# Performance work log

Measured on AMD Instinct MI355X. Metric: run time of the kernel, lower is better.

## Reference

```python
import jax, jax.numpy as jnp
import numpy as np

K3 = 27            # kernel_size**3
PAIRS_PER_K = 131072  # pairs per kernel offset (equal-size segments)
N_VOX = 262144     # active voxels (stride-1, same grid: N_in == N_out)
C_IN = 32
C_OUT = 32


def setup_inputs() -> dict:
    key = jax.random.key(0)
    k1, k2, k3, k4 = jax.random.split(key, 4)
    M = K3 * PAIRS_PER_K
    in_feature = jax.random.normal(k1, (N_VOX, C_IN), dtype=jnp.float32)
    kernel = jax.random.normal(k2, (K3, C_IN, C_OUT), dtype=jnp.float32) * (1.0 / np.sqrt(C_IN * K3))
    bias = jax.random.normal(k3, (C_OUT,), dtype=jnp.float32) * 0.01
    # nbmap[:, 0] = input voxel index, nbmap[:, 1] = output voxel index,
    # sorted by kernel offset (offset k owns rows [k*P, (k+1)*P)).
    nbmap = jax.random.randint(k4, (M, 2), 0, N_VOX, dtype=jnp.int32)
    nbsizes = jnp.full((K3,), PAIRS_PER_K, dtype=jnp.int32)
    return {"in_feature": in_feature, "kernel": kernel, "bias": bias,
            "nbmap": nbmap, "nbsizes": nbsizes}


def reference(in_feature, kernel, bias, nbmap, nbsizes):
    """Gather -> per-offset GEMM -> scatter-add, matching
    ext.conv.sparse_convolution for a stride-1 non-transposed conv where
    nbmap rows are grouped by kernel offset with equal segment sizes."""
    k3, c_in, c_out = kernel.shape
    m = nbmap.shape[0]
    p = m // k3  # pairs per offset (static)
    n_out = in_feature.shape[0]  # same grid, stride 1
    # gather input features for every (input, output) pair  [M, C_in]
    gathered = in_feature[nbmap[:, 0]]
    # batched GEMM: one [P, C_in] x [C_in, C_out] per kernel offset
    contrib = jnp.einsum('kpi,kio->kpo', gathered.reshape(k3, p, c_in), kernel)
    contrib = contrib.reshape(m, c_out)
    # scatter-add contributions into output voxels
    out = jax.ops.segment_sum(contrib, nbmap[:, 1], num_segments=n_out)
    return out + bias
```

## Files before the change

kernel.cpp:

```cpp
#include <hip/hip_runtime.h>
#include <hip/hip_bf16.h>


#define N_VOX    262144
#define LOG2_NV  18
#define C_CH     32
#define K3       27
#define LOG2_PPK 17
#define BLOCK    256
#define FLAG_FIN 0x40000000
#define ECAP     4096
#define PLPAD    36
#define FRAGN    (K3 * 2 * 64)

typedef __attribute__((ext_vector_type(8))) short bf16x8;
typedef __attribute__((ext_vector_type(4))) float f32x4;

__device__ __forceinline__ unsigned short f2bf(float f) {
  union { __hip_bfloat16 h; unsigned short u; } cv;
  cv.h = __float2bfloat16(f);
  return cv.u;
}

__global__ __launch_bounds__(BLOCK) void passA_kernel(
    const int4* __restrict__ nbmap2, int* __restrict__ T, int Mh) {
  int q = blockIdx.x * BLOCK + threadIdx.x;
  if (q >= Mh) return;
  int4 nb = nbmap2[q];
  int p0 = q << 1, p1 = (q << 1) | 1;
  T[((p0 >> LOG2_PPK) << LOG2_NV) + nb.y] = p0;
  T[((p1 >> LOG2_PPK) << LOG2_NV) + nb.w] = p1;
}

__device__ __forceinline__ void loser_path(
    int vox, int k, int in, int* __restrict__ T2, int idx, int use2,
    int* __restrict__ ovf_cnt, int* __restrict__ ovf, int S2,
    int* __restrict__ ecnt, int2* __restrict__ elist) {
  int val = in;
  if (use2) {
    val = atomicExch(&T2[idx], val);
    if (val < 0) return;
  }
  int pos = atomicAdd(&ovf_cnt[vox], 1);
  if (pos < S2) {
    ovf[(pos << LOG2_NV) + vox] = (k << LOG2_NV) | val;
  } else {
    int ep = atomicAdd(ecnt, 1);
    if (ep < ECAP) elist[ep] = make_int2(vox, (k << LOG2_NV) | val);
  }
}

__global__ __launch_bounds__(BLOCK) void passB_kernel(
    const int4* __restrict__ nbmap2, int* __restrict__ T, int* __restrict__ T2,
    int use2, int* __restrict__ ovf_cnt, int* __restrict__ ovf, int S2,
    int* __restrict__ ecnt, int2* __restrict__ elist, int Mh) {
  int q = blockIdx.x * BLOCK + threadIdx.x;
  if (q >= Mh) return;
  int4 nb = nbmap2[q];
  int p0 = q << 1, p1 = (q << 1) | 1;
  int k0 = p0 >> LOG2_PPK, k1 = p1 >> LOG2_PPK;
  int idx0 = (k0 << LOG2_NV) + nb.y;
  int idx1 = (k1 << LOG2_NV) + nb.w;
  int t0 = T[idx0];
  int t1 = T[idx1];
  if (t0 == p0) {
    T[idx0] = FLAG_FIN | nb.x;
  } else {
    loser_path(nb.y, k0, nb.x, T2, idx0, use2, ovf_cnt, ovf, S2, ecnt, elist);
  }
  if (t1 == p1) {
    T[idx1] = FLAG_FIN | nb.z;
  } else {
    loser_path(nb.w, k1, nb.z, T2, idx1, use2, ovf_cnt, ovf, S2, ecnt, elist);
  }
}

__global__ __launch_bounds__(BLOCK) void bf_prep_kernel(
    const float* __restrict__ kernel_w, unsigned short* __restrict__ Bf) {
  int tid = blockIdx.x * BLOCK + threadIdx.x;
  if (tid >= FRAGN) return;
  int lane = tid & 63;
  int kc = tid >> 6;
  int k = kc >> 1, t = kc & 1;
  int i0 = (lane >> 4) * 8;
  int c = t * 16 + (lane & 15);
  union { unsigned short u[8]; uint4 v; } pk;
#pragma unroll
  for (int j = 0; j < 8; ++j)
    pk.u[j] = f2bf(kernel_w[(k << 10) + (i0 + j) * C_CH + c]);
  ((uint4*)Bf)[tid] = pk.v;
}

__global__ __launch_bounds__(BLOCK) void feat16_prep_kernel(
    const float* __restrict__ in_feature, unsigned short* __restrict__ feat16) {
  int idx = blockIdx.x * BLOCK + threadIdx.x;
  const float4* src = (const float4*)in_feature + (idx << 1);
  float4 f0 = src[0], f1 = src[1];
  union { unsigned short u[8]; uint4 v; } pk;
  pk.u[0] = f2bf(f0.x); pk.u[1] = f2bf(f0.y);
  pk.u[2] = f2bf(f0.z); pk.u[3] = f2bf(f0.w);
  pk.u[4] = f2bf(f1.x); pk.u[5] = f2bf(f1.y);
  pk.u[6] = f2bf(f1.z); pk.u[7] = f2bf(f1.w);
  ((uint4*)feat16)[idx] = pk.v;
}

template <int F16>
__global__ __launch_bounds__(BLOCK, 4) void gather_splitk_kernel(
    const float* __restrict__ in_feature,
    const unsigned short* __restrict__ feat16,
    const float* __restrict__ kernel_w,
    const float* __restrict__ bias,
    const int* __restrict__ T,
    const int* __restrict__ T2, int use2,
    const int* __restrict__ ovf_cnt,
    const int* __restrict__ ovf,
    const unsigned short* __restrict__ Bf,
    float* __restrict__ out, int S2) {
  __shared__ float plane[4][16][PLPAD];
  __shared__ int flatE[256];
  __shared__ int scnt[16];

  const int tid = threadIdx.x;
  const int w = tid >> 6;
  const int lane = tid & 63;
  const int r16 = lane & 15;
  const int quad = lane >> 4;
  const int vb = blockIdx.x << 4;

  if (tid < 16) {
    int c = ovf_cnt[vb + tid];
    scnt[tid] = c < S2 ? c : S2;
  }
  __syncthreads();
  const int er = tid & 15;
  const int ej = tid >> 4;
  int myb = 0, tot = 0;
#pragma unroll
  for (int q = 0; q < 16; ++q) {
    int cq = scnt[q];
    if (q < er) myb += cq;
    tot += cq;
  }
  if (ej < scnt[er])
    flatE[myb + ej] = (er << 24) | ovf[(ej << LOG2_NV) + vb + er];
  __syncthreads();

  const int kb = w * 7;
  const int kn = (w == 3) ? 6 : 7;
  const int v = vb + r16;
  int tv[7], tv2[7];
#pragma unroll
  for (int d = 0; d < 7; ++d)
    tv[d] = (d < kn) ? T[((kb + d) << LOG2_NV) + v] : -1;
#pragma unroll
  for (int d = 0; d < 7; ++d)
    tv2[d] = (use2 && d < kn) ? T2[((kb + d) << LOG2_NV) + v] : -1;

  bf16x8 R0[7], R1[7];
#pragma unroll
  for (int d = 0; d < 7; ++d) {
    int t = tv[d];
    int in = (t >= 0) ? (t & 0x3FFFF) : 0;
    bf16x8 a;
    if (F16) {
      a = *reinterpret_cast<const bf16x8*>(feat16 + (in << 5) + (quad << 3));
    } else {
      const float4* ap = (const float4*)(in_feature + (in << 5) + (quad << 3));
      float4 f0 = ap[0], f1 = ap[1];
      a[0] = (short)f2bf(f0.x); a[1] = (short)f2bf(f0.y);
      a[2] = (short)f2bf(f0.z); a[3] = (short)f2bf(f0.w);
      a[4] = (short)f2bf(f1.x); a[5] = (short)f2bf(f1.y);
      a[6] = (short)f2bf(f1.z); a[7] = (short)f2bf(f1.w);
    }
    if (t < 0) a = (bf16x8)0;
    R0[d] = a;
  }
#pragma unroll
  for (int d = 0; d < 7; ++d) {
    int t = tv2[d];
    int in = (t >= 0) ? (t & 0x3FFFF) : 0;
    bf16x8 a;
    if (F16) {
      a = *reinterpret_cast<const bf16x8*>(feat16 + (in << 5) + (quad << 3));
    } else {
      const float4* ap = (const float4*)(in_feature + (in << 5) + (quad << 3));
      float4 f0 = ap[0], f1 = ap[1];
      a[0] = (short)f2bf(f0.x); a[1] = (short)f2bf(f0.y);
      a[2] = (short)f2bf(f0.z); a[3] = (short)f2bf(f0.w);
      a[4] = (short)f2bf(f1.x); a[5] = (short)f2bf(f1.y);
      a[6] = (short)f2bf(f1.z); a[7] = (short)f2bf(f1.w);
    }
    if (t < 0) a = (bf16x8)0;
    R1[d] = a;
  }

  f32x4 acc0 = {0.f, 0.f, 0.f, 0.f};
  f32x4 acc1 = {0.f, 0.f, 0.f, 0.f};
  const uint4* bfp = (const uint4*)Bf;
#pragma unroll
  for (int d = 0; d < 7; ++d) {
    if (d < kn) {
      int k = kb + d;
      uint4 h0 = bfp[(k * 2 + 0) * 64 + lane];
      uint4 h1 = bfp[(k * 2 + 1) * 64 + lane];
      acc0 = __builtin_amdgcn_mfma_f32_16x16x32_bf16(
          R0[d], *reinterpret_cast<const bf16x8*>(&h0), acc0, 0, 0, 0);
      acc1 = __builtin_amdgcn_mfma_f32_16x16x32_bf16(
          R0[d], *reinterpret_cast<const bf16x8*>(&h1), acc1, 0, 0, 0);
    }
  }
  if (use2) {
#pragma unroll
    for (int d = 0; d < 7; ++d) {
      if (d < kn) {
        int k = kb + d;
        uint4 h0 = bfp[(k * 2 + 0) * 64 + lane];
        uint4 h1 = bfp[(k * 2 + 1) * 64 + lane];
        acc0 = __builtin_amdgcn_mfma_f32_16x16x32_bf16(
            R1[d], *reinterpret_cast<const bf16x8*>(&h0), acc0, 0, 0, 0);
        acc1 = __builtin_amdgcn_mfma_f32_16x16x32_bf16(
            R1[d], *reinterpret_cast<const bf16x8*>(&h1), acc1, 0, 0, 0);
      }
    }
  }

#pragma unroll
  for (int reg = 0; reg < 4; ++reg) {
    int row = quad * 4 + reg;
    plane[w][row][r16] = acc0[reg];
    plane[w][row][16 + r16] = acc1[reg];
  }

  const int c32 = lane & 31, h = lane >> 5;
  int i = w;
  int e_cur = 0;
  float4 p0, p1, p2, p3;
  if (i < tot) {
    e_cur = flatE[i];
    const float4* ar =
        (const float4*)(in_feature + ((e_cur & 0x3FFFF) << 5) + (h << 4));
    p0 = ar[0]; p1 = ar[1]; p2 = ar[2]; p3 = ar[3];
  }
  while (i < tot) {
    const int e = e_cur;
    float4 q0 = p0, q1 = p1, q2 = p2, q3 = p3;
    const int inext = i + 4;
    if (inext < tot) {
      e_cur = flatE[inext];
      const float4* ar =
          (const float4*)(in_feature + ((e_cur & 0x3FFFF) << 5) + (h << 4));
      p0 = ar[0]; p1 = ar[1]; p2 = ar[2]; p3 = ar[3];
    }
    const int k2 = (e >> LOG2_NV) & 31;
    const int rr = (e >> 24) & 15;
    const float* wcol = kernel_w + (k2 << 10) + (h << 4) * C_CH + c32;
    float psum = 0.f;
    psum = fmaf(q0.x, wcol[0 * C_CH], psum);
    psum = fmaf(q0.y, wcol[1 * C_CH], psum);
    psum = fmaf(q0.z, wcol[2 * C_CH], psum);
    psum = fmaf(q0.w, wcol[3 * C_CH], psum);
    psum = fmaf(q1.x, wcol[4 * C_CH], psum);
    psum = fmaf(q1.y, wcol[5 * C_CH], psum);
    psum = fmaf(q1.z, wcol[6 * C_CH], psum);
    psum = fmaf(q1.w, wcol[7 * C_CH], psum);
    psum = fmaf(q2.x, wcol[8 * C_CH], psum);
    psum = fmaf(q2.y, wcol[9 * C_CH], psum);
    psum = fmaf(q2.z, wcol[10 * C_CH], psum);
    psum = fmaf(q2.w, wcol[11 * C_CH], psum);
    psum = fmaf(q3.x, wcol[12 * C_CH], psum);
    psum = fmaf(q3.y, wcol[13 * C_CH], psum);
    psum = fmaf(q3.z, wcol[14 * C_CH], psum);
    psum = fmaf(q3.w, wcol[15 * C_CH], psum);
    psum += __shfl_xor(psum, 32);
    if (h == 0) plane[w][rr][c32] += psum;
    i = inext;
  }

  __syncthreads();
  const int mr = tid >> 4;
  const int mc = (tid & 15) << 1;
  float s0 = plane[0][mr][mc] + plane[1][mr][mc] + plane[2][mr][mc] +
             plane[3][mr][mc] + bias[mc];
  float s1 = plane[0][mr][mc + 1] + plane[1][mr][mc + 1] +
             plane[2][mr][mc + 1] + plane[3][mr][mc + 1] + bias[mc + 1];
  float2 o; o.x = s0; o.y = s1;
  *(float2*)(out + ((vb + mr) << 5) + mc) = o;
}

__global__ __launch_bounds__(BLOCK) void emergency_kernel(
    const float* __restrict__ in_feature, const float* __restrict__ kernel_w,
    const int* __restrict__ ecnt, const int2* __restrict__ elist,
    float* __restrict__ out) {
  int e = blockIdx.x * BLOCK + threadIdx.x;
  int n = *ecnt;
  if (n > ECAP) n = ECAP;
  if (e >= n) return;
  int2 ent = elist[e];
  int v = ent.x, k = ent.y >> LOG2_NV, in = ent.y & 0x3FFFF;
  float a[C_CH];
  const float4* ar = (const float4*)(in_feature + (in << 5));
#pragma unroll
  for (int q = 0; q < 8; ++q) ((float4*)a)[q] = ar[q];
  for (int c = 0; c < C_CH; ++c) {
    float s = 0.f;
#pragma unroll
    for (int i = 0; i < C_CH; ++i)
      s = fmaf(a[i], kernel_w[(k << 10) + i * C_CH + c], s);
    atomicAdd(&out[v * C_CH + c], s);
  }
}

__global__ __launch_bounds__(BLOCK) void init_bias_kernel(
    float* __restrict__ out, const float* __restrict__ bias, int n4) {
  int idx = blockIdx.x * blockDim.x + threadIdx.x;
  if (idx >= n4) return;
  ((float4*)out)[idx] = ((const float4*)bias)[idx & 7];
}

__global__ __launch_bounds__(BLOCK) void scatter_conv_kernel(
    const float* __restrict__ in_feature, const float* __restrict__ kernel_w,
    const int* __restrict__ nbmap, float* __restrict__ out) {
  const int k = blockIdx.x >> 9;
  const int pair = blockIdx.x * BLOCK + threadIdx.x;
  const float* __restrict__ Wk = kernel_w + k * (C_CH * C_CH);
  const int2 nb = ((const int2*)nbmap)[pair];
  const float4* __restrict__ inrow =
      (const float4*)(in_feature + (long)nb.x * C_CH);
  float a[C_CH];
#pragma unroll
  for (int j = 0; j < 8; ++j) ((float4*)a)[j] = inrow[j];
  float acc[C_CH];
#pragma unroll
  for (int c = 0; c < C_CH; ++c) acc[c] = 0.0f;
#pragma unroll
  for (int i = 0; i < C_CH; ++i) {
    const float av = a[i];
#pragma unroll
    for (int c = 0; c < C_CH; ++c)
      acc[c] = fmaf(av, Wk[i * C_CH + c], acc[c]);
  }
  float* __restrict__ orow = out + (long)nb.y * C_CH;
#pragma unroll
  for (int c = 0; c < C_CH; ++c) atomicAdd(orow + c, acc[c]);
}

extern "C" void kernel_launch(void* const* d_in, const int* in_sizes, int n_in,
                              void* d_out, int out_size, void* d_ws,
                              size_t ws_size, hipStream_t stream) {
  const float* in_feature = (const float*)d_in[0];
  const float* kernel_w   = (const float*)d_in[1];
  const float* bias       = (const float*)d_in[2];
  const int*   nbmap      = (const int*)d_in[3];
  float* out = (float*)d_out;
  const int M = in_sizes[3] / 2;
  const int Mh = M / 2;

  const long FIXED = 64 + 2 * ECAP + 13824;
  long ws_ints = (long)(ws_size / 4);
  long planes = (ws_ints - FIXED) / N_VOX;
  int use2 = 0, use16 = 0;
  long s2c;
  if (planes >= 75) {
    use2 = 1; use16 = 1;
    s2c = planes - 71;
    if (s2c > 7) s2c = 7;
  } else if (planes >= 59) {
    use2 = 1;
    s2c = planes - 55;
    if (s2c > 7) s2c = 7;
  } else {
    s2c = planes - 28;
    if (s2c > 15) s2c = 15;
  }
  int S2 = (int)s2c;

  if (!use2 && S2 < 4) {
    const int n4 = out_size / 4;
    init_bias_kernel<<<(n4 + BLOCK - 1) / BLOCK, BLOCK, 0, stream>>>(out, bias,
                                                                     n4);
    scatter_conv_kernel<<<M / BLOCK, BLOCK, 0, stream>>>(in_feature, kernel_w,
                                                         nbmap, out);
    return;
  }

  const long TPLANES = (long)K3 * N_VOX;
  int* T        = (int*)d_ws;
  int* T2       = use2 ? (T + TPLANES) : T;
  int* ovf_cnt  = T + TPLANES * (1 + use2);
  int* ecnt     = ovf_cnt + N_VOX;
  int2* elist   = (int2*)(ecnt + 64);
  unsigned short* Bf = (unsigned short*)(ecnt + 64 + 2 * ECAP);
  int* ovf      = ((int*)Bf) + 13824;
  unsigned short* feat16 = (unsigned short*)(ovf + (long)S2 * N_VOX);

  hipMemsetAsync(T, 0xFF, (size_t)TPLANES * 4 * (1 + use2), stream);
  hipMemsetAsync(ovf_cnt, 0, (size_t)(N_VOX + 64) * 4, stream);

  bf_prep_kernel<<<(FRAGN + BLOCK - 1) / BLOCK, BLOCK, 0, stream>>>(kernel_w,
                                                                    Bf);
  if (use16)
    feat16_prep_kernel<<<(N_VOX * 4) / BLOCK, BLOCK, 0, stream>>>(in_feature,
                                                                  feat16);
  passA_kernel<<<(Mh + BLOCK - 1) / BLOCK, BLOCK, 0, stream>>>(
      (const int4*)nbmap, T, Mh);
  passB_kernel<<<(Mh + BLOCK - 1) / BLOCK, BLOCK, 0, stream>>>(
      (const int4*)nbmap, T, T2, use2, ovf_cnt, ovf, S2, ecnt, elist, Mh);
  if (use16)
    gather_splitk_kernel<1><<<N_VOX / 16, BLOCK, 0, stream>>>(
        in_feature, feat16, kernel_w, bias, T, T2, use2, ovf_cnt, ovf, Bf,
        out, S2);
  else
    gather_splitk_kernel<0><<<N_VOX / 16, BLOCK, 0, stream>>>(
        in_feature, feat16, kernel_w, bias, T, T2, use2, ovf_cnt, ovf, Bf,
        out, S2);
  emergency_kernel<<<ECAP / BLOCK, BLOCK, 0, stream>>>(in_feature, kernel_w,
                                                       ecnt, elist, out);
}
```

Before: 389.1 us.

## Fuse setup memsets and prep kernels, widen pass work, hoist gather loads

Two memsets and the bf16 weight and feature prep kernels become one setup kernel that clears the T planes and counters and converts features and weights, removing several launches. passA and passB now handle four pairs per thread instead of two, which gives more memory-level parallelism per thread and halves the thread count. In the gather kernel, the overflow-list load and the T-plane loads are issued before the first barrier so their latency overlaps the count reduction. Risks are a larger, divergent setup grid and more register pressure in the pass kernels.

```diff
diff --git a/kernel.cpp b/kernel.cpp
--- a/kernel.cpp
+++ b/kernel.cpp
@@ -12,6 +12,7 @@
 #define ECAP     4096
 #define PLPAD    36
 #define FRAGN    (K3 * 2 * 64)
+#define NF16     (N_VOX * 4)
 
 typedef __attribute__((ext_vector_type(8))) short bf16x8;
 typedef __attribute__((ext_vector_type(4))) float f32x4;
@@ -22,14 +23,62 @@
   return cv.u;
 }
 
+__global__ __launch_bounds__(BLOCK) void setup_kernel(
+    int4* __restrict__ clrT, long nt4, int4* __restrict__ clrC, long nc4,
+    const float* __restrict__ in_feature, unsigned short* __restrict__ feat16,
+    int use16, const float* __restrict__ kernel_w,
+    unsigned short* __restrict__ Bf) {
+  long idx = (long)blockIdx.x * BLOCK + threadIdx.x;
+  if (idx < nt4) {
+    clrT[idx] = make_int4(-1, -1, -1, -1);
+    return;
+  }
+  idx -= nt4;
+  if (idx < nc4) {
+    clrC[idx] = make_int4(0, 0, 0, 0);
+    return;
+  }
+  idx -= nc4;
+  if (use16) {
+    if (idx < NF16) {
+      const float4* src = (const float4*)in_feature + (idx << 1);
+      float4 f0 = src[0], f1 = src[1];
+      union { unsigned short u[8]; uint4 v; } pk;
+      pk.u[0] = f2bf(f0.x); pk.u[1] = f2bf(f0.y);
+      pk.u[2] = f2bf(f0.z); pk.u[3] = f2bf(f0.w);
+      pk.u[4] = f2bf(f1.x); pk.u[5] = f2bf(f1.y);
+      pk.u[6] = f2bf(f1.z); pk.u[7] = f2bf(f1.w);
+      ((uint4*)feat16)[idx] = pk.v;
+      return;
+    }
+    idx -= NF16;
+  }
+  if (idx < FRAGN) {
+    int wid = (int)idx;
+    int lane = wid & 63;
+    int kc = wid >> 6;
+    int k = kc >> 1, t = kc & 1;
+    int i0 = (lane >> 4) * 8;
+    int c = t * 16 + (lane & 15);
+    union { unsigned short u[8]; uint4 v; } pk;
+#pragma unroll
+    for (int j = 0; j < 8; ++j)
+      pk.u[j] = f2bf(kernel_w[(k << 10) + (i0 + j) * C_CH + c]);
+    ((uint4*)Bf)[wid] = pk.v;
+  }
+}
+
 __global__ __launch_bounds__(BLOCK) void passA_kernel(
-    const int4* __restrict__ nbmap2, int* __restrict__ T, int Mh) {
+    const int4* __restrict__ nbmap2, int* __restrict__ T, int Mq) {
   int q = blockIdx.x * BLOCK + threadIdx.x;
-  if (q >= Mh) return;
-  int4 nb = nbmap2[q];
-  int p0 = q << 1, p1 = (q << 1) | 1;
-  T[((p0 >> LOG2_PPK) << LOG2_NV) + nb.y] = p0;
-  T[((p1 >> LOG2_PPK) << LOG2_NV) + nb.w] = p1;
+  if (q >= Mq) return;
+  int4 na = nbmap2[q * 2];
+  int4 nb = nbmap2[q * 2 + 1];
+  int p0 = q << 2, p1 = p0 | 1, p2 = p0 | 2, p3 = p0 | 3;
+  T[((p0 >> LOG2_PPK) << LOG2_NV) + na.y] = p0;
+  T[((p1 >> LOG2_PPK) << LOG2_NV) + na.w] = p1;
+  T[((p2 >> LOG2_PPK) << LOG2_NV) + nb.y] = p2;
+  T[((p3 >> LOG2_PPK) << LOG2_NV) + nb.w] = p3;
 }
 
 __device__ __forceinline__ void loser_path(
@@ -53,55 +102,32 @@
 __global__ __launch_bounds__(BLOCK) void passB_kernel(
     const int4* __restrict__ nbmap2, int* __restrict__ T, int* __restrict__ T2,
     int use2, int* __restrict__ ovf_cnt, int* __restrict__ ovf, int S2,
-    int* __restrict__ ecnt, int2* __restrict__ elist, int Mh) {
+    int* __restrict__ ecnt, int2* __restrict__ elist, int Mq) {
   int q = blockIdx.x * BLOCK + threadIdx.x;
-  if (q >= Mh) return;
-  int4 nb = nbmap2[q];
-  int p0 = q << 1, p1 = (q << 1) | 1;
-  int k0 = p0 >> LOG2_PPK, k1 = p1 >> LOG2_PPK;
-  int idx0 = (k0 << LOG2_NV) + nb.y;
-  int idx1 = (k1 << LOG2_NV) + nb.w;
+  if (q >= Mq) return;
+  int4 na = nbmap2[q * 2];
+  int4 nb = nbmap2[q * 2 + 1];
+  int p0 = q << 2, p1 = p0 | 1, p2 = p0 | 2, p3 = p0 | 3;
+  int idx0 = ((p0 >> LOG2_PPK) << LOG2_NV) + na.y;
+  int idx1 = ((p1 >> LOG2_PPK) << LOG2_NV) + na.w;
+  int idx2 = ((p2 >> LOG2_PPK) << LOG2_NV) + nb.y;
+  int idx3 = ((p3 >> LOG2_PPK) << LOG2_NV) + nb.w;
   int t0 = T[idx0];
   int t1 = T[idx1];
-  if (t0 == p0) {
-    T[idx0] = FLAG_FIN | nb.x;
-  } else {
-    loser_path(nb.y, k0, nb.x, T2, idx0, use2, ovf_cnt, ovf, S2, ecnt, elist);
-  }
-  if (t1 == p1) {
-    T[idx1] = FLAG_FIN | nb.z;
-  } else {
-    loser_path(nb.w, k1, nb.z, T2, idx1, use2, ovf_cnt, ovf, S2, ecnt, elist);
-  }
-}
-
-__global__ __launch_bounds__(BLOCK) void bf_prep_kernel(
-    const float* __restrict__ kernel_w, unsigned short* __restrict__ Bf) {
-  int tid = blockIdx.x * BLOCK + threadIdx.x;
-  if (tid >= FRAGN) return;
-  int lane = tid & 63;
-  int kc = tid >> 6;
-  int k = kc >> 1, t = kc & 1;
-  int i0 = (lane >> 4) * 8;
-  int c = t * 16 + (lane & 15);
-  union { unsigned short u[8]; uint4 v; } pk;
-#pragma unroll
-  for (int j = 0; j < 8; ++j)
-    pk.u[j] = f2bf(kernel_w[(k << 10) + (i0 + j) * C_CH + c]);
-  ((uint4*)Bf)[tid] = pk.v;
-}
-
-__global__ __launch_bounds__(BLOCK) void feat16_prep_kernel(
-    const float* __restrict__ in_feature, unsigned short* __restrict__ feat16) {
-  int idx = blockIdx.x * BLOCK + threadIdx.x;
-  const float4* src = (const float4*)in_feature + (idx << 1);
-  float4 f0 = src[0], f1 = src[1];
-  union { unsigned short u[8]; uint4 v; } pk;
-  pk.u[0] = f2bf(f0.x); pk.u[1] = f2bf(f0.y);
-  pk.u[2] = f2bf(f0.z); pk.u[3] = f2bf(f0.w);
-  pk.u[4] = f2bf(f1.x); pk.u[5] = f2bf(f1.y);
-  pk.u[6] = f2bf(f1.z); pk.u[7] = f2bf(f1.w);
-  ((uint4*)feat16)[idx] = pk.v;
+  int t2 = T[idx2];
+  int t3 = T[idx3];
+  if (t0 == p0) T[idx0] = FLAG_FIN | na.x;
+  else loser_path(na.y, p0 >> LOG2_PPK, na.x, T2, idx0, use2, ovf_cnt, ovf,
+                  S2, ecnt, elist);
+  if (t1 == p1) T[idx1] = FLAG_FIN | na.z;
+  else loser_path(na.w, p1 >> LOG2_PPK, na.z, T2, idx1, use2, ovf_cnt, ovf,
+                  S2, ecnt, elist);
+  if (t2 == p2) T[idx2] = FLAG_FIN | nb.x;
+  else loser_path(nb.y, p2 >> LOG2_PPK, nb.x, T2, idx2, use2, ovf_cnt, ovf,
+                  S2, ecnt, elist);
+  if (t3 == p3) T[idx3] = FLAG_FIN | nb.z;
+  else loser_path(nb.w, p3 >> LOG2_PPK, nb.z, T2, idx3, use2, ovf_cnt, ovf,
+                  S2, ecnt, elist);
 }
 
 template <int F16>
@@ -127,13 +153,24 @@
   const int quad = lane >> 4;
   const int vb = blockIdx.x << 4;
 
+  const int er = tid & 15;
+  const int ej = tid >> 4;
+  int eval = 0;
+  if (ej < S2)
+    eval = ovf[(ej << LOG2_NV) + vb + er];
   if (tid < 16) {
     int c = ovf_cnt[vb + tid];
     scnt[tid] = c < S2 ? c : S2;
   }
+  const int kb = w * 7;
+  const int kn = (w == 3) ? 6 : 7;
+  const int v = vb + r16;
+  int tv[7];
+#pragma unroll
+  for (int d = 0; d < 7; ++d)
+    tv[d] = (d < kn) ? T[((kb + d) << LOG2_NV) + v] : -1;
   __syncthreads();
-  const int er = tid & 15;
-  const int ej = tid >> 4;
+
   int myb = 0, tot = 0;
 #pragma unroll
   for (int q = 0; q < 16; ++q) {
@@ -142,16 +179,10 @@
     tot += cq;
   }
   if (ej < scnt[er])
-    flatE[myb + ej] = (er << 24) | ovf[(ej << LOG2_NV) + vb + er];
+    flatE[myb + ej] = (er << 24) | eval;
   __syncthreads();
 
-  const int kb = w * 7;
-  const int kn = (w == 3) ? 6 : 7;
-  const int v = vb + r16;
-  int tv[7], tv2[7];
-#pragma unroll
-  for (int d = 0; d < 7; ++d)
-    tv[d] = (d < kn) ? T[((kb + d) << LOG2_NV) + v] : -1;
+  int tv2[7];
 #pragma unroll
   for (int d = 0; d < 7; ++d)
     tv2[d] = (use2 && d < kn) ? T2[((kb + d) << LOG2_NV) + v] : -1;
@@ -353,7 +384,7 @@
   const int*   nbmap      = (const int*)d_in[3];
   float* out = (float*)d_out;
   const int M = in_sizes[3] / 2;
-  const int Mh = M / 2;
+  const int Mq = M / 4;
 
   const long FIXED = 64 + 2 * ECAP + 13824;
   long ws_ints = (long)(ws_size / 4);
@@ -393,18 +424,18 @@
   int* ovf      = ((int*)Bf) + 13824;
   unsigned short* feat16 = (unsigned short*)(ovf + (long)S2 * N_VOX);
 
-  hipMemsetAsync(T, 0xFF, (size_t)TPLANES * 4 * (1 + use2), stream);
-  hipMemsetAsync(ovf_cnt, 0, (size_t)(N_VOX + 64) * 4, stream);
-
-  bf_prep_kernel<<<(FRAGN + BLOCK - 1) / BLOCK, BLOCK, 0, stream>>>(kernel_w,
-                                                                    Bf);
-  if (use16)
-    feat16_prep_kernel<<<(N_VOX * 4) / BLOCK, BLOCK, 0, stream>>>(in_feature,
-                                                                  feat16);
-  passA_kernel<<<(Mh + BLOCK - 1) / BLOCK, BLOCK, 0, stream>>>(
-      (const int4*)nbmap, T, Mh);
-  passB_kernel<<<(Mh + BLOCK - 1) / BLOCK, BLOCK, 0, stream>>>(
-      (const int4*)nbmap, T, T2, use2, ovf_cnt, ovf, S2, ecnt, elist, Mh);
+  const long nt4 = TPLANES * (1 + use2) / 4;
+  const long nc4 = (N_VOX + 64) / 4;
+  const long total = nt4 + nc4 + (use16 ? (long)NF16 : 0) + FRAGN;
+  const long sblocks = (total + BLOCK - 1) / BLOCK;
+  setup_kernel<<<(int)sblocks, BLOCK, 0, stream>>>(
+      (int4*)T, nt4, (int4*)ovf_cnt, nc4, in_feature, feat16, use16, kernel_w,
+      Bf);
+
+  passA_kernel<<<(Mq + BLOCK - 1) / BLOCK, BLOCK, 0, stream>>>(
+      (const int4*)nbmap, T, Mq);
+  passB_kernel<<<(Mq + BLOCK - 1) / BLOCK, BLOCK, 0, stream>>>(
+      (const int4*)nbmap, T, T2, use2, ovf_cnt, ovf, S2, ecnt, elist, Mq);
   if (use16)
     gather_splitk_kernel<1><<<N_VOX / 16, BLOCK, 0, stream>>>(
         in_feature, feat16, kernel_w, bias, T, T2, use2, ovf_cnt, ovf, Bf,
```

Result: no change. 393.9 us (+1.3%).
